# Optimization experiments

Hardware: AMD Instinct MI355X
Metric: run time of the kernel (lower is better)

## Reference

```python
import jax, jax.numpy as jnp
import numpy as np

B, S, D, H, DFF = 2, 2048, 1024, 16, 4096
DH = D // H
EPS = 1e-5


def setup_inputs() -> dict:
    key = jax.random.key(0)
    ks = jax.random.split(key, 12)
    s = 0.02
    x = jax.random.normal(ks[0], (B, S, D), dtype=jnp.float32)
    # causal decoder mask, True = keep
    mask = jnp.tril(jnp.ones((S, S), dtype=bool))[None, None, :, :]
    Wq = jax.random.normal(ks[1], (D, D), dtype=jnp.float32) * s
    Wk = jax.random.normal(ks[2], (D, D), dtype=jnp.float32) * s
    Wv = jax.random.normal(ks[3], (D, D), dtype=jnp.float32) * s
    Wo = jax.random.normal(ks[4], (D, D), dtype=jnp.float32) * s
    w1 = jax.random.normal(ks[5], (D, DFF), dtype=jnp.float32) * s
    b1 = jnp.zeros((DFF,), dtype=jnp.float32)
    w2 = jax.random.normal(ks[6], (DFF, D), dtype=jnp.float32) * s
    b2 = jnp.zeros((D,), dtype=jnp.float32)
    g1 = jnp.ones((D,), dtype=jnp.float32)
    be1 = jnp.zeros((D,), dtype=jnp.float32)
    g2 = jnp.ones((D,), dtype=jnp.float32)
    be2 = jnp.zeros((D,), dtype=jnp.float32)
    return dict(x=x, mask=mask, Wq=Wq, Wk=Wk, Wv=Wv, Wo=Wo,
                w1=w1, b1=b1, w2=w2, b2=b2, g1=g1, be1=be1, g2=g2, be2=be2)


def _layer_norm(x, gamma, beta):
    mu = jnp.mean(x, axis=-1, keepdims=True)
    var = jnp.mean(jnp.square(x - mu), axis=-1, keepdims=True)
    return (x - mu) * jax.lax.rsqrt(var + EPS) * gamma + beta


def _attention(x, mask, Wq, Wk, Wv, Wo):
    # x: [B,S,D] -> q,k,v: [B,H,S,DH]
    def split_heads(t):
        return t.reshape(x.shape[0], x.shape[1], H, DH).transpose(0, 2, 1, 3)
    q = split_heads(x @ Wq)
    k = split_heads(x @ Wk)
    v = split_heads(x @ Wv)
    scores = jnp.einsum('bhqd,bhkd->bhqk', q, k) / jnp.sqrt(jnp.float32(DH))
    scores = jnp.where(mask, scores, jnp.float32(-1e9))
    probs = jax.nn.softmax(scores, axis=-1)
    out = jnp.einsum('bhqk,bhkd->bhqd', probs, v)  # [B,H,S,DH]
    out = out.transpose(0, 2, 1, 3).reshape(x.shape[0], x.shape[1], -1)
    return out @ Wo


def reference(x, mask, Wq, Wk, Wv, Wo, w1, b1, w2, b2, g1, be1, g2, be2):
    # residual 1: pre-norm self-attention (dropout=0)
    h = x + _attention(_layer_norm(x, g1, be1), mask, Wq, Wk, Wv, Wo)
    # residual 2: pre-norm FFN
    hn = _layer_norm(h, g2, be2)
    ffn = jax.nn.relu(hn @ w1 + b1) @ w2 + b2
    return h + ffn
```

## Files before the change

### kernel.cpp

```cpp
#include <hip/hip_runtime.h>

typedef unsigned short u16;
typedef __attribute__((ext_vector_type(8))) short short8;
typedef __attribute__((ext_vector_type(4))) float f32x4;

#define CB 2
#define CS 2048
#define CD 1024
#define CH 16
#define CDH 64
#define CDFF 4096
#define NQB (CS / 64)

__device__ __forceinline__ u16 f2bf(float f){
  union { float f; unsigned u; } x; x.f = f;
  unsigned r = (x.u + 0x7fffu + ((x.u >> 16) & 1u)) >> 16;
  return (u16)r;
}

__device__ __forceinline__ u16 f2bf_pos(float f){
  union { float f; unsigned u; } x; x.f = f;
  return (u16)((x.u + 0x8000u) >> 16);
}

__device__ __forceinline__ void gload_lds16(const void* g, void* l){
  __builtin_amdgcn_global_load_lds(
    (const __attribute__((address_space(1))) void*)(unsigned long long)g,
    (__attribute__((address_space(3))) void*)(unsigned long long)l,
    16, 0, 0);
}


struct TPAll { const float* s[6]; u16* d[6]; };

__global__ __launch_bounds__(256)
void prep_all(TPAll p, const float* __restrict__ x, const float* __restrict__ g1,
              const float* __restrict__ be1, u16* __restrict__ yln)
{
  const int g = blockIdx.x >> 12;
  const int id = blockIdx.x & 4095;
  const int tid = threadIdx.x;

  if (g == 3){
    const int row = id;
    const int lane = tid & 63, wave = tid >> 6;
    const float4 v = ((const float4*)(x + (size_t)row * CD))[tid];
    float s  = v.x + v.y + v.z + v.w;
    float s2 = v.x*v.x + v.y*v.y + v.z*v.z + v.w*v.w;
    #pragma unroll
    for (int m = 1; m < 64; m <<= 1){ s += __shfl_xor(s, m); s2 += __shfl_xor(s2, m); }
    __shared__ float red[8];
    if (lane == 0){ red[wave] = s; red[4 + wave] = s2; }
    __syncthreads();
    s  = red[0] + red[1] + red[2] + red[3];
    s2 = red[4] + red[5] + red[6] + red[7];
    const float mu = s * (1.0f / CD);
    const float var = s2 * (1.0f / CD) - mu * mu;
    const float rs = rsqrtf(var + 1e-5f);
    const float4 gv = ((const float4*)g1)[tid];
    const float4 bv = ((const float4*)be1)[tid];
    ushort4 o;
    o.x = f2bf((v.x - mu) * rs * gv.x + bv.x);
    o.y = f2bf((v.y - mu) * rs * gv.y + bv.y);
    o.z = f2bf((v.z - mu) * rs * gv.z + bv.z);
    o.w = f2bf((v.w - mu) * rs * gv.w + bv.w);
    ((ushort4*)yln)[(size_t)row * (CD / 4) + tid] = o;
    return;
  }

  __shared__ float t[32][33];
  const float* __restrict__ in;
  u16* __restrict__ out;
  int K, N, n0, k0;
  if (g == 0){
    const int w = id >> 10, tile = id & 1023;
    in = p.s[w]; out = p.d[w]; K = 1024; N = 1024;
    n0 = (tile & 31) * 32; k0 = (tile >> 5) * 32;
  } else if (g == 1){
    in = p.s[4]; out = p.d[4]; K = 1024; N = 4096;
    n0 = (id & 127) * 32; k0 = (id >> 7) * 32;
  } else {
    in = p.s[5]; out = p.d[5]; K = 4096; N = 1024;
    n0 = (id & 31) * 32; k0 = (id >> 5) * 32;
  }
  const int c = tid & 31, r4 = tid >> 5;
  #pragma unroll
  for (int i = 0; i < 4; i++){
    int r = r4 + i * 8;
    t[r][c] = in[(size_t)(k0 + r) * N + n0 + c];
  }
  __syncthreads();
  #pragma unroll
  for (int i = 0; i < 4; i++){
    int r = r4 + i * 8;
    out[(size_t)(n0 + r) * K + k0 + c] = f2bf(t[c][r]);
  }
}

template<int MODE>
__global__ __launch_bounds__(256)
void ln_bf16(const float* __restrict__ xin, const float* __restrict__ g,
             const float* __restrict__ be, u16* __restrict__ outp,
             float4* __restrict__ aux, const float* __restrict__ bias)
{
  const int row = blockIdx.x, tid = threadIdx.x;
  const int lane = tid & 63, wave = tid >> 6;
  const float4 v = ((const float4*)(xin + (size_t)row * CD))[tid];
  float s  = v.x + v.y + v.z + v.w;
  float s2 = v.x*v.x + v.y*v.y + v.z*v.z + v.w*v.w;
  #pragma unroll
  for (int m = 1; m < 64; m <<= 1){ s += __shfl_xor(s, m); s2 += __shfl_xor(s2, m); }
  __shared__ float red[8];
  if (lane == 0){ red[wave] = s; red[4 + wave] = s2; }

  if (MODE == 2){
    const float4 b4 = ((const float4*)bias)[tid];
    float4 w = v;
    w.x += b4.x; w.y += b4.y; w.z += b4.z; w.w += b4.w;
    aux[(size_t)row * 256 + tid] = w;
  }

  __syncthreads();
  s  = red[0] + red[1] + red[2] + red[3];
  s2 = red[4] + red[5] + red[6] + red[7];
  const float mu = s * (1.0f / CD);
  const float var = s2 * (1.0f / CD) - mu * mu;
  const float rs = rsqrtf(var + 1e-5f);
  const float4 gv = ((const float4*)g)[tid];
  const float4 bv = ((const float4*)be)[tid];
  ushort4 o;
  o.x = f2bf((v.x - mu) * rs * gv.x + bv.x);
  o.y = f2bf((v.y - mu) * rs * gv.y + bv.y);
  o.z = f2bf((v.z - mu) * rs * gv.z + bv.z);
  o.w = f2bf((v.w - mu) * rs * gv.w + bv.w);
  ((ushort4*)outp)[(size_t)row * (CD / 4) + tid] = o;
}

template<int EPI>
__global__ __launch_bounds__(256)
void gemm_bt(const u16* __restrict__ A, const u16* __restrict__ Bt,
             void* __restrict__ Cout, const float* __restrict__ bias,
             int M, int N, int K,
             int ldc, int vsplit, u16* __restrict__ vtout)
{
  __shared__ __align__(16) u16 lA[128 * 64];
  __shared__ __align__(16) u16 lB[128 * 64];
  const int tid = threadIdx.x;
  const int wave = tid >> 6, lane = tid & 63;

  const int G = gridDim.x;
  const int flat = blockIdx.x;
  const int t = (flat & 7) * (G >> 3) + (flat >> 3);
  const int NN = N >> 7;
  const int n_i = t % NN;
  const int m_i = t / NN;

  const int m0 = m_i * 128, n0 = n_i * 128;
  const int wm = (wave >> 1) * 64, wn = (wave & 1) * 64;
  const int lq = lane >> 4, lr = lane & 15;
  const int l7 = lr & 7;
  const int sw0 = ((lq ^ l7) << 3);
  const int sw1 = (((4 + lq) ^ l7) << 3);

  f32x4 acc[4][4] = {};

  const u16* Ab = A + (size_t)m0 * K;
  const u16* Bb = Bt + (size_t)n0 * K;
  const int srow = lane >> 3;
  const int scol = (((lane & 7) ^ srow)) * 8;

  auto stage = [&](int k0){
    #pragma unroll
    for (int i = 0; i < 4; i++){
      const int c = i * 4 + wave;
      const int row = c * 8 + srow;
      gload_lds16(Ab + (size_t)row * K + k0 + scol, &lA[c * 512]);
      gload_lds16(Bb + (size_t)row * K + k0 + scol, &lB[c * 512]);
    }
  };

  const int nit = K >> 6;
  stage(0);
  for (int i = 0; i < nit; i++){
    asm volatile("s_waitcnt vmcnt(0)\n\ts_barrier" ::: "memory");
    #pragma unroll
    for (int kh = 0; kh < 2; kh++){
      const int sw = kh ? sw1 : sw0;
      short8 aF[4], bF[4];
      #pragma unroll
      for (int i2 = 0; i2 < 4; i2++) aF[i2] = *(const short8*)&lA[(wm + i2 * 16 + lr) * 64 + sw];
      #pragma unroll
      for (int j = 0; j < 4; j++) bF[j] = *(const short8*)&lB[(wn + j * 16 + lr) * 64 + sw];
      #pragma unroll
      for (int i2 = 0; i2 < 4; i2++)
        #pragma unroll
        for (int j = 0; j < 4; j++)
          acc[i2][j] = __builtin_amdgcn_mfma_f32_16x16x32_bf16(aF[i2], bF[j], acc[i2][j], 0, 0, 0);
    }
    asm volatile("s_barrier" ::: "memory");
    if (i + 1 < nit) stage((i + 1) * 64);
  }

  if (EPI == 0 && n0 >= vsplit){
    #pragma unroll
    for (int i = 0; i < 4; i++){
      const int row0 = m0 + wm + i * 16 + lq * 4;
      const int bb = row0 >> 11, s = row0 & 2047;
      #pragma unroll
      for (int j = 0; j < 4; j++){
        const int col = n0 - vsplit + wn + j * 16 + lr;
        ushort4 o;
        o.x = f2bf(acc[i][j][0]); o.y = f2bf(acc[i][j][1]);
        o.z = f2bf(acc[i][j][2]); o.w = f2bf(acc[i][j][3]);
        *(ushort4*)&vtout[((size_t)(bb * 1024 + col)) * CS + s] = o;
      }
    }
    return;
  }

  const float osc = (EPI == 0 && n0 < 1024) ? 0.125f : 1.0f;

  #pragma unroll
  for (int i = 0; i < 4; i++){
    const int row = m0 + wm + i * 16 + lq * 4;
    #pragma unroll
    for (int j = 0; j < 4; j++){
      const int col = n0 + wn + j * 16 + lr;
      #pragma unroll
      for (int r = 0; r < 4; r++){
        float v = acc[i][j][r];
        const size_t off = (size_t)(row + r) * ldc + col;
        if (EPI == 0){
          ((u16*)Cout)[off] = f2bf(v * osc);
        } else {
          v += bias[col]; v = v > 0.0f ? v : 0.0f;
          ((u16*)Cout)[off] = f2bf(v);
        }
      }
    }
  }
}

__global__ __launch_bounds__(256)
void gemm_bt64(const u16* __restrict__ A, const u16* __restrict__ Bt,
               const float* __restrict__ resid, float* __restrict__ Cout,
               int M, int N, int K)
{
  __shared__ __align__(16) u16 lA[2][64 * 64];
  __shared__ __align__(16) u16 lB[2][128 * 64];
  const int tid = threadIdx.x;
  const int wave = tid >> 6, lane = tid & 63;

  const int G = gridDim.x;
  const int flat = blockIdx.x;
  const int t = (flat & 7) * (G >> 3) + (flat >> 3);
  const int NN = N >> 7;
  const int n_i = t % NN;
  const int m_i = t / NN;
  const int m0 = m_i * 64, n0 = n_i * 128;
  const int lq = lane >> 4, lr = lane & 15;
  const int l7 = lr & 7;
  const int sw0 = ((lq ^ l7) << 3);
  const int sw1 = (((4 + lq) ^ l7) << 3);

  f32x4 acc[4][2] = {};

  const u16* Ab = A + (size_t)m0 * K;
  const u16* Bb = Bt + (size_t)n0 * K;
  const int srow = lane >> 3;
  const int scol = (((lane & 7) ^ srow)) * 8;

  auto stage = [&](int buf, int kt){
    const int k0 = kt * 64;
    #pragma unroll
    for (int i = 0; i < 6; i++){
      const int c = i * 4 + wave;
      if (c < 8){
        gload_lds16(Ab + (size_t)(c * 8 + srow) * K + k0 + scol, &lA[buf][c * 512]);
      } else {
        const int cb2 = c - 8;
        gload_lds16(Bb + (size_t)(cb2 * 8 + srow) * K + k0 + scol, &lB[buf][cb2 * 512]);
      }
    }
  };

  const int nit = K >> 6;
  stage(0, 0);
  for (int i = 0; i < nit; i++){
    const int cb = i & 1;
    if (i + 1 < nit){
      stage(cb ^ 1, i + 1);
      asm volatile("s_waitcnt vmcnt(6)\n\ts_barrier" ::: "memory");
    } else {
      asm volatile("s_waitcnt vmcnt(0)\n\ts_barrier" ::: "memory");
    }
    #pragma unroll
    for (int kh = 0; kh < 2; kh++){
      const int sw = kh ? sw1 : sw0;
      short8 aF[4], bF[2];
      #pragma unroll
      for (int i2 = 0; i2 < 4; i2++) aF[i2] = *(const short8*)&lA[cb][(i2 * 16 + lr) * 64 + sw];
      #pragma unroll
      for (int j = 0; j < 2; j++) bF[j] = *(const short8*)&lB[cb][(wave * 32 + j * 16 + lr) * 64 + sw];
      #pragma unroll
      for (int i2 = 0; i2 < 4; i2++)
        #pragma unroll
        for (int j = 0; j < 2; j++)
          acc[i2][j] = __builtin_amdgcn_mfma_f32_16x16x32_bf16(aF[i2], bF[j], acc[i2][j], 0, 0, 0);
    }
    asm volatile("s_barrier" ::: "memory");
  }

  #pragma unroll
  for (int i = 0; i < 4; i++){
    const int row = m0 + i * 16 + lq * 4;
    #pragma unroll
    for (int j = 0; j < 2; j++){
      const int col = n0 + wave * 32 + j * 16 + lr;
      #pragma unroll
      for (int r = 0; r < 4; r++){
        const size_t off = (size_t)(row + r) * N + col;
        Cout[off] = resid[off] + acc[i][j][r];
      }
    }
  }
}

__global__ __launch_bounds__(256)
void attn_kernel(const u16* __restrict__ qk, const u16* __restrict__ vt,
                 u16* __restrict__ outp)
{
  __shared__ __align__(16) u16 lK[2][64 * 64];
  __shared__ __align__(16) u16 lVt[2][64 * 64];
  __shared__ __align__(16) u16 lP[4][16 * 72];
  const int tid = threadIdx.x, wave = tid >> 6, lane = tid & 63;
  const int lq = lane >> 4, lr = lane & 15;
  const int l7 = lr & 7;
  const int sw0 = ((lq ^ l7) << 3);
  const int sw1 = (((4 + lq) ^ l7) << 3);
  const int bh = blockIdx.x, b = bh >> 4, h = bh & 15;
  const int RS = 2048;
  const int srow = lane >> 3;
  const int scol = (((lane & 7) ^ srow)) * 8;

  const size_t kbase = (size_t)(b * CS) * RS + 1024 + h * CDH;
  const size_t vbase = (size_t)(bh * CDH) * CS;
  u16* lPw = lP[wave];

  auto stageKV = [&](int buf, int kt){
    #pragma unroll
    for (int cc = 0; cc < 2; cc++){
      const int c = wave * 2 + cc;
      gload_lds16(qk + kbase + (size_t)(kt * 64 + c * 8 + srow) * RS + scol, &lK[buf][c * 512]);
      gload_lds16(vt + vbase + (size_t)(c * 8 + srow) * CS + kt * 64 + scol, &lVt[buf][c * 512]);
    }
  };

  const int iq = (NQB - 1) - blockIdx.y;
  const int q0 = iq * 64;
  const int ktmax = iq + 1;

  const int qrow = b * CS + q0 + wave * 16 + lr;
  const u16* qp = qk + (size_t)qrow * RS + h * CDH;
  const short8 qf0 = *(const short8*)(qp + lq * 8);
  const short8 qf1 = *(const short8*)(qp + 32 + lq * 8);

  f32x4 o[4] = {};
  float lsum[4] = {0.0f, 0.0f, 0.0f, 0.0f};

  stageKV(0, 0);
  for (int kt = 0; kt < ktmax; ++kt){
    const int cb = kt & 1;
    if (kt + 1 < ktmax){
      stageKV(cb ^ 1, kt + 1);
      asm volatile("s_waitcnt vmcnt(4)\n\ts_barrier" ::: "memory");
    } else {
      asm volatile("s_waitcnt vmcnt(0)\n\ts_barrier" ::: "memory");
    }

    f32x4 s[4] = {};
    #pragma unroll
    for (int nb = 0; nb < 4; nb++){
      const short8 bk0 = *(const short8*)&lK[cb][(nb * 16 + lr) * 64 + sw0];
      const short8 bk1 = *(const short8*)&lK[cb][(nb * 16 + lr) * 64 + sw1];
      s[nb] = __builtin_amdgcn_mfma_f32_16x16x32_bf16(qf0, bk0, s[nb], 0, 0, 0);
      s[nb] = __builtin_amdgcn_mfma_f32_16x16x32_bf16(qf1, bk1, s[nb], 0, 0, 0);
    }

    const bool diag = (kt + 1) == ktmax;
    const int qg = q0 + wave * 16 + lq * 4;
    #pragma unroll
    for (int r = 0; r < 4; r++){
      float e0 = __expf(s[0][r]);
      float e1 = __expf(s[1][r]);
      float e2 = __expf(s[2][r]);
      float e3 = __expf(s[3][r]);
      if (diag){
        const int q = qg + r, kb = kt * 64 + lr;
        e0 = (kb      <= q) ? e0 : 0.0f;
        e1 = (kb + 16 <= q) ? e1 : 0.0f;
        e2 = (kb + 32 <= q) ? e2 : 0.0f;
        e3 = (kb + 48 <= q) ? e3 : 0.0f;
      }
      lsum[r] += (e0 + e1) + (e2 + e3);
      const int prow = (lq * 4 + r) * 72;
      lPw[prow + lr]      = f2bf_pos(e0);
      lPw[prow + 16 + lr] = f2bf_pos(e1);
      lPw[prow + 32 + lr] = f2bf_pos(e2);
      lPw[prow + 48 + lr] = f2bf_pos(e3);
    }

    asm volatile("s_waitcnt lgkmcnt(0)" ::: "memory");
    const short8 pf0 = *(const short8*)&lPw[lr * 72 + lq * 8];
    const short8 pf1 = *(const short8*)&lPw[lr * 72 + 32 + lq * 8];

    #pragma unroll
    for (int nb = 0; nb < 4; nb++){
      const short8 bv0 = *(const short8*)&lVt[cb][(nb * 16 + lr) * 64 + sw0];
      const short8 bv1 = *(const short8*)&lVt[cb][(nb * 16 + lr) * 64 + sw1];
      o[nb] = __builtin_amdgcn_mfma_f32_16x16x32_bf16(pf0, bv0, o[nb], 0, 0, 0);
      o[nb] = __builtin_amdgcn_mfma_f32_16x16x32_bf16(pf1, bv1, o[nb], 0, 0, 0);
    }
    asm volatile("s_barrier" ::: "memory");
  }

  #pragma unroll
  for (int r = 0; r < 4; r++){
    float l = lsum[r];
    l += __shfl_xor(l, 1);
    l += __shfl_xor(l, 2);
    l += __shfl_xor(l, 4);
    l += __shfl_xor(l, 8);
    const float inv = __builtin_amdgcn_rcpf(l);
    const size_t row = (size_t)(b * CS + q0 + wave * 16 + lq * 4 + r);
    #pragma unroll
    for (int nb = 0; nb < 4; nb++)
      outp[row * CD + h * CDH + nb * 16 + lr] = f2bf(o[nb][r] * inv);
  }
}

extern "C" void kernel_launch(void* const* d_in, const int* in_sizes, int n_in,
                              void* d_out, int out_size, void* d_ws, size_t ws_size,
                              hipStream_t stream)
{
  const float* x   = (const float*)d_in[0];
  const float* Wq  = (const float*)d_in[2];
  const float* Wk  = (const float*)d_in[3];
  const float* Wv  = (const float*)d_in[4];
  const float* Wo  = (const float*)d_in[5];
  const float* w1  = (const float*)d_in[6];
  const float* b1  = (const float*)d_in[7];
  const float* w2  = (const float*)d_in[8];
  const float* b2  = (const float*)d_in[9];
  const float* g1  = (const float*)d_in[10];
  const float* be1 = (const float*)d_in[11];
  const float* g2  = (const float*)d_in[12];
  const float* be2 = (const float*)d_in[13];
  float* out = (float*)d_out;

  char* ws = (char*)d_ws;
  const size_t MB = 1u << 20;
  u16* yln    = (u16*)(ws);
  u16* qk     = (u16*)(ws + 8  * MB);
  u16* vt     = (u16*)(ws + 24 * MB);
  u16* attn   = (u16*)(ws + 32 * MB);
  u16* mid    = (u16*)(ws + 40 * MB);
  u16* Wqkv_t = (u16*)(ws + 72 * MB);
  u16* Wo_t   = (u16*)(ws + 78 * MB);
  u16* w1_t   = (u16*)(ws + 80 * MB);
  u16* w2_t   = (u16*)(ws + 88 * MB);

  const int M = CB * CS;
  const int BIG = 1 << 30;

  TPAll pa;
  pa.s[0] = Wq; pa.s[1] = Wk; pa.s[2] = Wv; pa.s[3] = Wo; pa.s[4] = w1; pa.s[5] = w2;
  pa.d[0] = Wqkv_t;
  pa.d[1] = Wqkv_t + (size_t)CD * CD;
  pa.d[2] = Wqkv_t + (size_t)2 * CD * CD;
  pa.d[3] = Wo_t;
  pa.d[4] = w1_t;
  pa.d[5] = w2_t;
  prep_all<<<4 * 4096, 256, 0, stream>>>(pa, x, g1, be1, yln);

  gemm_bt<0><<<24 * 32, 256, 0, stream>>>(yln, Wqkv_t, qk, nullptr, M, 3 * CD, CD, 2048, 2048, vt);
  attn_kernel<<<dim3(CB * CH, NQB), 256, 0, stream>>>(qk, vt, attn);
  gemm_bt64<<<64 * 8, 256, 0, stream>>>(attn, Wo_t, x, out, M, CD, CD);
  ln_bf16<2><<<M, 256, 0, stream>>>(out, g2, be2, yln, (float4*)out, b2);
  gemm_bt<1><<<32 * 32, 256, 0, stream>>>(yln, w1_t, mid, b1, M, CDFF, CD, CDFF, BIG, nullptr);
  gemm_bt64<<<64 * 8, 256, 0, stream>>>(mid, w2_t, out, out, M, CD, CDFF);
}
```

Baseline: 311.9 us.

## Use 256x256 tiles with double-buffered staggered prefetch in bf16 GEMM

Rewrites the QKV and FFN-up GEMM kernel to use 256x256 output tiles with 512 threads (8 waves, each computing 128x64). A/B tiles are double-buffered in LDS, and global-to-LDS loads for the next k-tiles are interleaved across quarter-iterations, with partial vmcnt waits and s_setprio around MFMA bursts. The goal is to overlap memory with compute and raise arithmetic intensity per block. In exchange it uses 128 KB of LDS and more accumulator registers, and the grid shrinks to 192/256 blocks, which may underfill the GPU's CUs.

```diff
diff --git a/kernel.cpp b/kernel.cpp
--- a/kernel.cpp
+++ b/kernel.cpp
@@ -137,81 +137,130 @@
 }
 
 template<int EPI>
-__global__ __launch_bounds__(256)
+__global__ __launch_bounds__(512)
 void gemm_bt(const u16* __restrict__ A, const u16* __restrict__ Bt,
              void* __restrict__ Cout, const float* __restrict__ bias,
              int M, int N, int K,
              int ldc, int vsplit, u16* __restrict__ vtout)
 {
-  __shared__ __align__(16) u16 lA[128 * 64];
-  __shared__ __align__(16) u16 lB[128 * 64];
+  __shared__ __align__(16) u16 sA[2][2][128 * 64];
+  __shared__ __align__(16) u16 sB[2][2][128 * 64];
   const int tid = threadIdx.x;
   const int wave = tid >> 6, lane = tid & 63;
+  const int wm = wave >> 2, wn = wave & 3;
 
   const int G = gridDim.x;
   const int flat = blockIdx.x;
-  const int t = (flat & 7) * (G >> 3) + (flat >> 3);
-  const int NN = N >> 7;
-  const int n_i = t % NN;
-  const int m_i = t / NN;
-
-  const int m0 = m_i * 128, n0 = n_i * 128;
-  const int wm = (wave >> 1) * 64, wn = (wave & 1) * 64;
+  const int t0_ = (flat & 7) * (G >> 3) + (flat >> 3);
+  const int NN = N >> 8;
+  const int n_i = t0_ % NN;
+  const int m_i = t0_ / NN;
+
+  const int m0 = m_i * 256, n0 = n_i * 256;
   const int lq = lane >> 4, lr = lane & 15;
   const int l7 = lr & 7;
   const int sw0 = ((lq ^ l7) << 3);
   const int sw1 = (((4 + lq) ^ l7) << 3);
 
-  f32x4 acc[4][4] = {};
+  f32x4 acc[8][4] = {};
 
   const u16* Ab = A + (size_t)m0 * K;
   const u16* Bb = Bt + (size_t)n0 * K;
   const int srow = lane >> 3;
   const int scol = (((lane & 7) ^ srow)) * 8;
 
-  auto stage = [&](int k0){
-    #pragma unroll
-    for (int i = 0; i < 4; i++){
-      const int c = i * 4 + wave;
-      const int row = c * 8 + srow;
-      gload_lds16(Ab + (size_t)row * K + k0 + scol, &lA[c * 512]);
-      gload_lds16(Bb + (size_t)row * K + k0 + scol, &lB[c * 512]);
+  auto stageA = [&](int par, int h, int kt){
+    const u16* src = Ab + (size_t)(h * 128) * K + kt * 64;
+    u16* dst = &sA[par][h][0];
+    #pragma unroll
+    for (int i = 0; i < 2; i++){
+      const int c = wave * 2 + i;
+      gload_lds16(src + (size_t)(c * 8 + srow) * K + scol, dst + c * 512);
     }
   };
-
-  const int nit = K >> 6;
-  stage(0);
-  for (int i = 0; i < nit; i++){
-    asm volatile("s_waitcnt vmcnt(0)\n\ts_barrier" ::: "memory");
-    #pragma unroll
-    for (int kh = 0; kh < 2; kh++){
-      const int sw = kh ? sw1 : sw0;
-      short8 aF[4], bF[4];
-      #pragma unroll
-      for (int i2 = 0; i2 < 4; i2++) aF[i2] = *(const short8*)&lA[(wm + i2 * 16 + lr) * 64 + sw];
-      #pragma unroll
-      for (int j = 0; j < 4; j++) bF[j] = *(const short8*)&lB[(wn + j * 16 + lr) * 64 + sw];
-      #pragma unroll
-      for (int i2 = 0; i2 < 4; i2++)
+  auto stageB = [&](int par, int h, int kt){
+    const u16* src = Bb + (size_t)(h * 128) * K + kt * 64;
+    u16* dst = &sB[par][h][0];
+    #pragma unroll
+    for (int i = 0; i < 2; i++){
+      const int c = wave * 2 + i;
+      gload_lds16(src + (size_t)(c * 8 + srow) * K + scol, dst + c * 512);
+    }
+  };
+
+  const int nt = K >> 6;
+
+  stageB(0, 0, 0); stageB(0, 1, 0);
+  stageA(0, 0, 0); stageA(0, 1, 0);
+  stageB(1, 0, 1); stageB(1, 1, 1);
+  asm volatile("s_waitcnt vmcnt(4)\n\ts_barrier" ::: "memory");
+
+  short8 bF0[4], bF1[4];
+
+  for (int t = 0; t < nt; t++){
+    const int par = t & 1;
+    const u16* aT = &sA[par][wm][0];
+    const u16* bT = &sB[par][wn >> 1][0];
+    const int bbase = (wn & 1) * 64;
+
+    #pragma unroll
+    for (int tq = 0; tq < 4; tq++){
+      if (tq == 0){
         #pragma unroll
-        for (int j = 0; j < 4; j++)
-          acc[i2][j] = __builtin_amdgcn_mfma_f32_16x16x32_bf16(aF[i2], bF[j], acc[i2][j], 0, 0, 0);
-    }
-    asm volatile("s_barrier" ::: "memory");
-    if (i + 1 < nit) stage((i + 1) * 64);
+        for (int j = 0; j < 4; j++){
+          bF0[j] = *(const short8*)&bT[(bbase + j * 16 + lr) * 64 + sw0];
+          bF1[j] = *(const short8*)&bT[(bbase + j * 16 + lr) * 64 + sw1];
+        }
+      }
+      const short8 a00 = *(const short8*)&aT[((tq * 2 + 0) * 16 + lr) * 64 + sw0];
+      const short8 a01 = *(const short8*)&aT[((tq * 2 + 0) * 16 + lr) * 64 + sw1];
+      const short8 a10 = *(const short8*)&aT[((tq * 2 + 1) * 16 + lr) * 64 + sw0];
+      const short8 a11 = *(const short8*)&aT[((tq * 2 + 1) * 16 + lr) * 64 + sw1];
+
+      if (tq == 0){ if (t + 1 < nt) stageA(par ^ 1, 0, t + 1); }
+      if (tq == 1){ if (t + 1 < nt) stageA(par ^ 1, 1, t + 1); }
+      if (tq == 2){ if (t + 2 < nt) stageB(par, 0, t + 2); }
+      if (tq == 3){ if (t + 2 < nt) stageB(par, 1, t + 2); }
+
+      asm volatile("s_barrier" ::: "memory");
+      asm volatile("s_waitcnt lgkmcnt(0)" ::: "memory");
+      __builtin_amdgcn_sched_barrier(0);
+
+      __builtin_amdgcn_s_setprio(1);
+      #pragma unroll
+      for (int j = 0; j < 4; j++){
+        acc[tq * 2 + 0][j] = __builtin_amdgcn_mfma_f32_16x16x32_bf16(a00, bF0[j], acc[tq * 2 + 0][j], 0, 0, 0);
+        acc[tq * 2 + 0][j] = __builtin_amdgcn_mfma_f32_16x16x32_bf16(a01, bF1[j], acc[tq * 2 + 0][j], 0, 0, 0);
+        acc[tq * 2 + 1][j] = __builtin_amdgcn_mfma_f32_16x16x32_bf16(a10, bF0[j], acc[tq * 2 + 1][j], 0, 0, 0);
+        acc[tq * 2 + 1][j] = __builtin_amdgcn_mfma_f32_16x16x32_bf16(a11, bF1[j], acc[tq * 2 + 1][j], 0, 0, 0);
+      }
+      __builtin_amdgcn_s_setprio(0);
+
+      if (tq == 3){
+        if (t == nt - 2){
+          asm volatile("s_waitcnt vmcnt(0)\n\ts_barrier" ::: "memory");
+        } else if (t < nt - 2){
+          asm volatile("s_waitcnt vmcnt(4)\n\ts_barrier" ::: "memory");
+        } else {
+          asm volatile("s_barrier" ::: "memory");
+        }
+      } else {
+        asm volatile("s_barrier" ::: "memory");
+      }
+    }
   }
 
   if (EPI == 0 && n0 >= vsplit){
     #pragma unroll
-    for (int i = 0; i < 4; i++){
-      const int row0 = m0 + wm + i * 16 + lq * 4;
+    for (int mf = 0; mf < 8; mf++){
+      const int row0 = m0 + wm * 128 + mf * 16 + lq * 4;
       const int bb = row0 >> 11, s = row0 & 2047;
       #pragma unroll
-      for (int j = 0; j < 4; j++){
-        const int col = n0 - vsplit + wn + j * 16 + lr;
+      for (int nf = 0; nf < 4; nf++){
+        const int col = n0 - vsplit + wn * 64 + nf * 16 + lr;
         ushort4 o;
-        o.x = f2bf(acc[i][j][0]); o.y = f2bf(acc[i][j][1]);
-        o.z = f2bf(acc[i][j][2]); o.w = f2bf(acc[i][j][3]);
+        o.x = f2bf(acc[mf][nf][0]); o.y = f2bf(acc[mf][nf][1]);
+        o.z = f2bf(acc[mf][nf][2]); o.w = f2bf(acc[mf][nf][3]);
         *(ushort4*)&vtout[((size_t)(bb * 1024 + col)) * CS + s] = o;
       }
     }
@@ -221,14 +270,14 @@
   const float osc = (EPI == 0 && n0 < 1024) ? 0.125f : 1.0f;
 
   #pragma unroll
-  for (int i = 0; i < 4; i++){
-    const int row = m0 + wm + i * 16 + lq * 4;
-    #pragma unroll
-    for (int j = 0; j < 4; j++){
-      const int col = n0 + wn + j * 16 + lr;
+  for (int mf = 0; mf < 8; mf++){
+    const int row = m0 + wm * 128 + mf * 16 + lq * 4;
+    #pragma unroll
+    for (int nf = 0; nf < 4; nf++){
+      const int col = n0 + wn * 64 + nf * 16 + lr;
       #pragma unroll
       for (int r = 0; r < 4; r++){
-        float v = acc[i][j][r];
+        float v = acc[mf][nf][r];
         const size_t off = (size_t)(row + r) * ldc + col;
         if (EPI == 0){
           ((u16*)Cout)[off] = f2bf(v * osc);
@@ -483,10 +532,10 @@
   pa.d[5] = w2_t;
   prep_all<<<4 * 4096, 256, 0, stream>>>(pa, x, g1, be1, yln);
 
-  gemm_bt<0><<<24 * 32, 256, 0, stream>>>(yln, Wqkv_t, qk, nullptr, M, 3 * CD, CD, 2048, 2048, vt);
+  gemm_bt<0><<<192, 512, 0, stream>>>(yln, Wqkv_t, qk, nullptr, M, 3 * CD, CD, 2048, 2048, vt);
   attn_kernel<<<dim3(CB * CH, NQB), 256, 0, stream>>>(qk, vt, attn);
   gemm_bt64<<<64 * 8, 256, 0, stream>>>(attn, Wo_t, x, out, M, CD, CD);
   ln_bf16<2><<<M, 256, 0, stream>>>(out, g2, be2, yln, (float4*)out, b2);
-  gemm_bt<1><<<32 * 32, 256, 0, stream>>>(yln, w1_t, mid, b1, M, CDFF, CD, CDFF, BIG, nullptr);
+  gemm_bt<1><<<256, 512, 0, stream>>>(yln, w1_t, mid, b1, M, CDFF, CD, CDFF, BIG, nullptr);
   gemm_bt64<<<64 * 8, 256, 0, stream>>>(mid, w2_t, out, out, M, CD, CDFF);
 }
```

New measurement: 313.9 us. No clear change (+0.7%).
